# Kernel tuning notes

Hardware: AMD Instinct MI355X
Metric: run time of the kernel (lower is better)

## Reference

```python
import jax, jax.numpy as jnp
import numpy as np

KK = 10.0  # sigmoid sharpness constant `kk` from the source

def sigmoid_k(x):
    return jax.nn.sigmoid(KK * x)

def setup_inputs() -> dict:
    key = jax.random.key(0)
    k1, k2, k3 = jax.random.split(key, 3)
    B, L = 8192, 4096
    # contiguous valid-prefix padding mask with random per-row lengths in [L//4, L)
    lens = jax.random.randint(k1, (B,), L // 4, L)
    mask = (jnp.arange(L)[None, :] < lens[:, None]).astype(jnp.float32)
    t = jax.random.uniform(k2, (B, 1), dtype=jnp.float32) * L          # crop centers
    l = 1.0 + jax.random.uniform(k3, (B, 1), dtype=jnp.float32) * (L / 2.0)  # half-widths
    return {"t": t, "l": l, "mask": mask, "length": L}

def reference(t, l, mask, length):
    t = t.reshape(-1, 1)
    l = l.reshape(-1, 1)
    # boundaries of the valid region (replaces the CPU numpy argmax round-trip)
    left = (jnp.argmax(mask, axis=-1).astype(jnp.float32) - 1.0)[:, None]          # [B,1]
    right = (float(length) - jnp.argmax(mask[:, ::-1], axis=-1).astype(jnp.float32))[:, None]  # [B,1]
    sentence_length = jnp.sum(mask, axis=-1, keepdims=True) / 2.0                   # [B,1]
    l_eff = jnp.where(l <= sentence_length, sentence_length, l)
    t_left = (t - l_eff) * (t - l_eff >= left).astype(jnp.float32)
    t_left = jnp.where(t_left == 0.0, left, t_left)
    t_right = ((t + l_eff) <= right).astype(jnp.float32) * (t + l_eff)
    t_right = jnp.where(t_right == 0.0, right, t_right)
    pos = jnp.arange(length, dtype=jnp.float32)                                     # [L]
    crop_mask = sigmoid_k(pos - t_left) - sigmoid_k(pos - t_right)                  # [B,L]
    crop_mask = (crop_mask >= 0.5).astype(jnp.float32) * mask
    return crop_mask
```

## Files before the change

### kernel.cpp

```cpp
#include <hip/hip_runtime.h>
#include <hip/hip_bf16.h>
#include <climits>


#define BLOCK 256

__device__ __forceinline__ float sigmoid10(float x) {
    return 1.0f / (1.0f + expf(-10.0f * x));
}
__device__ __forceinline__ float fdiff(float p, float tl, float tr) {
    return sigmoid10(p - tl) - sigmoid10(p - tr);
}

__global__ __launch_bounds__(BLOCK) void probe_kernel(
    const float* __restrict__ t, const float* __restrict__ l,
    const float* __restrict__ mask, int2* __restrict__ ws, int B, int Llen) {
    const int row = blockIdx.x * (BLOCK / 64) + (threadIdx.x >> 6);
    const int lane = threadIdx.x & 63;
    if (row >= B) return;

    const float* mrow = mask + (size_t)row * Llen;

    const int stride = (Llen + 63) >> 6;
    const int pos = lane * stride;
    const float m1 = (pos < Llen) ? mrow[pos] : 0.0f;
    const unsigned long long b1 = __ballot(m1 > 0.5f);
    const int z = __popcll(b1);

    int len = 0;
    if (z > 0) {
        const int base = (z - 1) * stride;
        const int p2 = base + 1 + lane;
        const float m2 = (lane < stride && p2 < Llen) ? mrow[p2] : 0.0f;
        const unsigned long long b2 = __ballot(m2 > 0.5f);
        len = base + 1 + __popcll(b2);
    }

    if (lane == 0) {
        int lo = 1, hi = 0;
        if (len > 0) {
            const float leftf  = -1.0f;
            const float rightf = (float)len;
            const float sl = 0.5f * (float)len;
            const float tv = t[row], lv = l[row];
            const float leff = (lv <= sl) ? sl : lv;
            float tl0 = tv - leff;
            float t_left = (tl0 >= leftf) ? tl0 : 0.0f;
            if (t_left == 0.0f) t_left = leftf;
            float tr0 = tv + leff;
            float t_right = (tr0 <= rightf) ? tr0 : 0.0f;
            if (t_right == 0.0f) t_right = rightf;

            const float c = expf(-10.0f * (t_right - t_left));
            const float b = 1.0f - 3.0f * c;
            const float disc = b * b - 4.0f * c;
            if (b > 0.0f && disc >= 0.0f) {
                const float xp = 0.5f * (b + sqrtf(disc));
                const float p_lo = t_left - 0.1f * logf(xp);
                const float p_hi = (t_left + t_right) - p_lo;
                lo = (int)ceilf(p_lo);
                hi = (int)floorf(p_hi);
                #pragma unroll 1
                for (int k = 0; k < 4 && fdiff((float)(lo - 1), t_left, t_right) >= 0.5f; ++k) --lo;
                #pragma unroll 1
                for (int k = 0; k < 4 && fdiff((float)lo, t_left, t_right) < 0.5f; ++k) ++lo;
                #pragma unroll 1
                for (int k = 0; k < 4 && fdiff((float)(hi + 1), t_left, t_right) >= 0.5f; ++k) ++hi;
                #pragma unroll 1
                for (int k = 0; k < 4 && fdiff((float)hi, t_left, t_right) < 0.5f; ++k) --hi;
            }
            lo = max(lo, 0);
            hi = min(hi, len - 1);
        }
        ws[row] = make_int2(lo, hi);
    }
}

__global__ __launch_bounds__(BLOCK) void emit_kernel(
    const int2* __restrict__ ws, float* __restrict__ out, int Llen) {
    const int row = blockIdx.x;
    const int2 bnd = ws[row];
    const int lo = bnd.x, hi = bnd.y;

    float4* orow = (float4*)(out + (size_t)row * Llen);
    const int nvec = Llen >> 2;
    for (int j = threadIdx.x; j < nvec; j += BLOCK) {
        const int e = j << 2;
        float4 o;
        o.x = (e     >= lo && e     <= hi) ? 1.0f : 0.0f;
        o.y = (e + 1 >= lo && e + 1 <= hi) ? 1.0f : 0.0f;
        o.z = (e + 2 >= lo && e + 2 <= hi) ? 1.0f : 0.0f;
        o.w = (e + 3 >= lo && e + 3 <= hi) ? 1.0f : 0.0f;
        orow[j] = o;
    }
}

extern "C" void kernel_launch(void* const* d_in, const int* in_sizes, int n_in,
                              void* d_out, int out_size, void* d_ws, size_t ws_size,
                              hipStream_t stream) {
    const float* t    = (const float*)d_in[0];
    const float* l    = (const float*)d_in[1];
    const float* mask = (const float*)d_in[2];
    float* out = (float*)d_out;
    int2* ws = (int2*)d_ws;

    const int B = in_sizes[0];
    const int Llen = in_sizes[2] / B;

    const int rows_per_block = BLOCK / 64;
    probe_kernel<<<(B + rows_per_block - 1) / rows_per_block, BLOCK, 0, stream>>>(
        t, l, mask, ws, B, Llen);
    emit_kernel<<<B, BLOCK, 0, stream>>>(ws, out, Llen);
}
```

Before: 241.2 us.

## Fuse probe and emit into one persistent wave-per-row kernel with ballot boundary search

Merges the boundary-probe kernel and the output-emit kernel into a single grid-stride kernel where each wave handles one row at a time. This removes the second launch and the workspace round-trip. Serial lane-0 boundary refinement is replaced by a parallel ballot over 24 candidate positions on each side. The output write per row is now done by one wave instead of a 256-thread block, which may reduce write parallelism per row but keeps the total store traffic the same.

```diff
diff --git a/kernel.cpp b/kernel.cpp
--- a/kernel.cpp
+++ b/kernel.cpp
@@ -4,6 +4,7 @@
 
 
 #define BLOCK 256
+#define WPB (BLOCK / 64)
 
 __device__ __forceinline__ float sigmoid10(float x) {
     return 1.0f / (1.0f + expf(-10.0f * x));
@@ -12,31 +13,31 @@
     return sigmoid10(p - tl) - sigmoid10(p - tr);
 }
 
-__global__ __launch_bounds__(BLOCK) void probe_kernel(
+__global__ __launch_bounds__(BLOCK) void crop_kernel(
     const float* __restrict__ t, const float* __restrict__ l,
-    const float* __restrict__ mask, int2* __restrict__ ws, int B, int Llen) {
-    const int row = blockIdx.x * (BLOCK / 64) + (threadIdx.x >> 6);
+    const float* __restrict__ mask, float* __restrict__ out,
+    int B, int Llen, int total_waves) {
     const int lane = threadIdx.x & 63;
-    if (row >= B) return;
+    const int wave0 = blockIdx.x * WPB + (threadIdx.x >> 6);
 
-    const float* mrow = mask + (size_t)row * Llen;
+    for (int row = wave0; row < B; row += total_waves) {
+        const float* mrow = mask + (size_t)row * Llen;
 
-    const int stride = (Llen + 63) >> 6;
-    const int pos = lane * stride;
-    const float m1 = (pos < Llen) ? mrow[pos] : 0.0f;
-    const unsigned long long b1 = __ballot(m1 > 0.5f);
-    const int z = __popcll(b1);
+        const int stride = (Llen + 63) >> 6;
+        const int pos = lane * stride;
+        const float m1 = (pos < Llen) ? mrow[pos] : 0.0f;
+        const unsigned long long b1 = __ballot(m1 > 0.5f);
+        const int z = __popcll(b1);
 
-    int len = 0;
-    if (z > 0) {
-        const int base = (z - 1) * stride;
-        const int p2 = base + 1 + lane;
-        const float m2 = (lane < stride && p2 < Llen) ? mrow[p2] : 0.0f;
-        const unsigned long long b2 = __ballot(m2 > 0.5f);
-        len = base + 1 + __popcll(b2);
-    }
+        int len = 0;
+        if (z > 0) {
+            const int base = (z - 1) * stride;
+            const int p2 = base + 1 + lane;
+            const float m2 = (lane < stride && p2 < Llen) ? mrow[p2] : 0.0f;
+            const unsigned long long b2 = __ballot(m2 > 0.5f);
+            len = base + 1 + __popcll(b2);
+        }
 
-    if (lane == 0) {
         int lo = 1, hi = 0;
         if (len > 0) {
             const float leftf  = -1.0f;
@@ -58,40 +59,34 @@
                 const float xp = 0.5f * (b + sqrtf(disc));
                 const float p_lo = t_left - 0.1f * logf(xp);
                 const float p_hi = (t_left + t_right) - p_lo;
-                lo = (int)ceilf(p_lo);
-                hi = (int)floorf(p_hi);
-                #pragma unroll 1
-                for (int k = 0; k < 4 && fdiff((float)(lo - 1), t_left, t_right) >= 0.5f; ++k) --lo;
-                #pragma unroll 1
-                for (int k = 0; k < 4 && fdiff((float)lo, t_left, t_right) < 0.5f; ++k) ++lo;
-                #pragma unroll 1
-                for (int k = 0; k < 4 && fdiff((float)(hi + 1), t_left, t_right) >= 0.5f; ++k) ++hi;
-                #pragma unroll 1
-                for (int k = 0; k < 4 && fdiff((float)hi, t_left, t_right) < 0.5f; ++k) --hi;
+                const int lo0 = (int)ceilf(p_lo);
+                const int hi0 = (int)floorf(p_hi);
+                int cand;
+                if (lane < 24)      cand = lo0 - 8 + lane;
+                else if (lane < 48) cand = hi0 - 8 + (lane - 24);
+                else                cand = lo0;
+                const bool ok = fdiff((float)cand, t_left, t_right) >= 0.5f;
+                const unsigned long long bm = __ballot(ok);
+                const unsigned int mlo = (unsigned int)(bm & 0xFFFFFFull);
+                const unsigned int mhi = (unsigned int)((bm >> 24) & 0xFFFFFFull);
+                lo = mlo ? (lo0 - 8 + (__ffs(mlo) - 1)) : (lo0 + 16);
+                hi = mhi ? (hi0 - 8 + (31 - __clz(mhi))) : (hi0 - 9);
             }
             lo = max(lo, 0);
             hi = min(hi, len - 1);
         }
-        ws[row] = make_int2(lo, hi);
-    }
-}
 
-__global__ __launch_bounds__(BLOCK) void emit_kernel(
-    const int2* __restrict__ ws, float* __restrict__ out, int Llen) {
-    const int row = blockIdx.x;
-    const int2 bnd = ws[row];
-    const int lo = bnd.x, hi = bnd.y;
-
-    float4* orow = (float4*)(out + (size_t)row * Llen);
-    const int nvec = Llen >> 2;
-    for (int j = threadIdx.x; j < nvec; j += BLOCK) {
-        const int e = j << 2;
-        float4 o;
-        o.x = (e     >= lo && e     <= hi) ? 1.0f : 0.0f;
-        o.y = (e + 1 >= lo && e + 1 <= hi) ? 1.0f : 0.0f;
-        o.z = (e + 2 >= lo && e + 2 <= hi) ? 1.0f : 0.0f;
-        o.w = (e + 3 >= lo && e + 3 <= hi) ? 1.0f : 0.0f;
-        orow[j] = o;
+        float4* orow = (float4*)(out + (size_t)row * Llen);
+        const int nvec = Llen >> 2;
+        for (int j = lane; j < nvec; j += 64) {
+            const int e = j << 2;
+            float4 o;
+            o.x = (e     >= lo && e     <= hi) ? 1.0f : 0.0f;
+            o.y = (e + 1 >= lo && e + 1 <= hi) ? 1.0f : 0.0f;
+            o.z = (e + 2 >= lo && e + 2 <= hi) ? 1.0f : 0.0f;
+            o.w = (e + 3 >= lo && e + 3 <= hi) ? 1.0f : 0.0f;
+            orow[j] = o;
+        }
     }
 }
 
@@ -102,13 +97,11 @@
     const float* l    = (const float*)d_in[1];
     const float* mask = (const float*)d_in[2];
     float* out = (float*)d_out;
-    int2* ws = (int2*)d_ws;
 
     const int B = in_sizes[0];
     const int Llen = in_sizes[2] / B;
 
-    const int rows_per_block = BLOCK / 64;
-    probe_kernel<<<(B + rows_per_block - 1) / rows_per_block, BLOCK, 0, stream>>>(
-        t, l, mask, ws, B, Llen);
-    emit_kernel<<<B, BLOCK, 0, stream>>>(ws, out, Llen);
+    const int blocks = 1024;
+    const int total_waves = blocks * WPB;
+    crop_kernel<<<blocks, BLOCK, 0, stream>>>(t, l, mask, out, B, Llen, total_waves);
 }
```

Measured after the change: 228.4 us. 5.3% less time.
